# Performance work log

Measured on AMD Instinct MI355X. Metric: run time of the kernel, lower is better.

Reference implementation:

```python
import jax, jax.numpy as jnp
import numpy as np

# Mex config (matches init_kwargs)
B, C, H, W = 64, 64, 64, 64
BLK = (64, 3, 3)        # block over (C, H, W); spans all channels -> out_c = 1
STR = (64, 2, 2)
PAD = (0, 1, 1)
NI = 256                # num_instances
EPS = 1.0
SOFTMAX_MODE = False    # False -> mean (logsumexp - log k), True -> plain logsumexp


def setup_inputs() -> dict:
    key = jax.random.key(0)
    k1, k2 = jax.random.split(key)
    x = jax.random.normal(k1, (B, C, H, W), dtype=jnp.float32)
    kblk = BLK[0] * BLK[1] * BLK[2]
    # Dirichlet([1]*k) init == normalized exponentials; nregions = 1 (shared offsets)
    e = jax.random.exponential(k2, (1, NI, kblk), dtype=jnp.float32)
    offsets = (e / jnp.sum(e, axis=-1, keepdims=True)).reshape(1, NI, *BLK)
    return {"x": x, "offsets": offsets}


def _mex_forward(x, offsets):
    eps = jnp.float32(EPS)
    bc, bh, bw = BLK
    # im2col patch extraction: (B, C*bh*bw, OH, OW); feature dim ordered (c, fh, fw)
    patches = jax.lax.conv_general_dilated_patches(
        x, (bh, bw), (STR[1], STR[2]),
        [(PAD[1], PAD[1]), (PAD[2], PAD[2])],  # zero padding == blocks_out_of_bounds_value
        dimension_numbers=("NCHW", "OIHW", "NCHW"),
    )
    Bn, K, OH, OW = patches.shape  # K = bc*bh*bw = 576
    P = patches.transpose(0, 2, 3, 1).reshape(-1, K)  # (N, k), N = B*OH*OW
    O = offsets.reshape(NI, K)                         # single shared region

    # y_ni = (1/eps) * logsumexp_k( eps*(P_nk + O_ik) ) - log(k)/eps (mean mode)
    # exp-domain GEMM with max-shift for stability:
    Pe = eps * P
    Oe = eps * O
    mp = jnp.max(Pe, axis=1, keepdims=True)   # (N, 1)
    mo = jnp.max(Oe, axis=1, keepdims=True)   # (I, 1)
    S = jnp.exp(Pe - mp) @ jnp.exp(Oe - mo).T  # (N, I)
    y = (jnp.log(S) + mp + mo.T) / eps
    if not SOFTMAX_MODE:
        y = y - jnp.log(jnp.float32(K)) / eps
    # output: (B, num_instances * out_c, OH, OW) with out_c = 1
    return y.reshape(Bn, OH, OW, NI).transpose(0, 3, 1, 2)


def reference(x, offsets):
    return _mex_forward(x, offsets)
```

## Files before the change

### kernel.cpp

```cpp
#include <hip/hip_runtime.h>
#include <hip/hip_bf16.h>


typedef __bf16 bf16x8 __attribute__((ext_vector_type(8)));
typedef float  f32x4  __attribute__((ext_vector_type(4)));

__global__ void mex_prep_b(const float* __restrict__ off, __bf16* __restrict__ Bt) {
    const int i = blockIdx.x * 4 + (threadIdx.x >> 6);
    const int c = threadIdx.x & 63;
    const int c8 = c >> 3, j = c & 7;
    const int wv = i >> 6, nt = (i >> 4) & 3, t16 = i & 15;
    const int q  = c8 & 3;
    const float* oi = off + i * 576;
    #pragma unroll
    for (int p = 0; p < 9; ++p) {
        float v = oi[c * 9 + p];
        const int ks    = p * 2 + (c8 >> 2);
        const int chunk = (ks * 16 + wv * 4 + nt) * 64 + q * 16 + t16;
        Bt[chunk * 8 + j] = (__bf16)__expf(v);
    }
}

__global__ __launch_bounds__(256, 2) void mex_main(
        const float* __restrict__ x,
        const __bf16* __restrict__ Bt,
        float* __restrict__ out) {
    __shared__ bf16x8 lds8[2 * 2560];

    const int bid = blockIdx.x;
    const int wid  = ((bid & 7) << 6) | (bid >> 3);
    const int b    = wid >> 3;
    const int j2   = wid & 7;
    const int oh0a = j2 << 2;
    const int oh0b = oh0a + 2;
    const int tid  = threadIdx.x;
    const int wv   = tid >> 6;
    const int lane = tid & 63;

    bf16x8 one8;
    #pragma unroll
    for (int j = 0; j < 8; ++j) one8[j] = (__bf16)1.0f;

    if (oh0a == 0) {
        #pragma unroll
        for (int i = 0; i < 2; ++i) lds8[tid + i * 256] = one8;
    }

    const int wp  = tid & 31;
    const int w0  = wp << 1;
    const int c8  = tid >> 5;
    const int c8p = c8 ^ (wp & 7);
    const float* xb = x + ((size_t)b << 18) + w0;

    #pragma unroll
    for (int hl = 0; hl < 5; ++hl) {
        const int hg = 2 * oh0a - 1 + hl;
        if (hg >= 0) {
            const float* xp = xb + (hg << 6);
            float2 v[8];
            #pragma unroll
            for (int k = 0; k < 8; ++k)
                v[k] = *(const float2*)(xp + (((c8 << 3) + k) << 12));
            bf16x8 ca, cb;
            #pragma unroll
            for (int k = 0; k < 8; ++k) {
                ca[k] = (__bf16)__expf(v[k].x);
                cb[k] = (__bf16)__expf(v[k].y);
            }
            bf16x8* dst = lds8 + hl * 512 + w0 * 8 + c8p;
            dst[0] = ca;
            dst[8] = cb;
        }
    }

    float2 v1[40];
    #pragma unroll
    for (int hl = 0; hl < 5; ++hl) {
        const int hg = 2 * oh0b - 1 + hl;
        const float* xp = xb + (hg << 6);
        #pragma unroll
        for (int k = 0; k < 8; ++k)
            v1[hl * 8 + k] = *(const float2*)(xp + (((c8 << 3) + k) << 12));
    }

    const bf16x8* __restrict__ Btv = (const bf16x8*)Bt;
    const int wv4 = wv << 2;
    bf16x8 b0[4], b1[4];
    #pragma unroll
    for (int nt = 0; nt < 4; ++nt) {
        b0[nt] = Btv[(wv4 + nt) * 64 + lane];
        b1[nt] = Btv[(16 + wv4 + nt) * 64 + lane];
    }

    const int t16 = tid & 15;
    const int q   = (tid >> 4) & 3;
    int hb[4], wo2[4];
    #pragma unroll
    for (int mt = 0; mt < 4; ++mt) {
        const int m = mt * 16 + t16;
        wo2[mt] = (m & 31) << 1;
        hb[mt]  = (m >> 5) << 7;
    }
    const float lK = 6.356107660695891f;

    auto kloop = [&](const bf16x8* __restrict__ L, f32x4 (&acc)[4][4],
                     bf16x8 (&bc)[4], bf16x8 (&bn)[4]) {
        #pragma unroll
        for (int ks = 0; ks < 18; ++ks) {
            const int p  = ks >> 1;
            const int fh = (p * 11) >> 5;
            const int fw = p - fh * 3;
            const int ccq = ((ks & 1) << 2) + q;
            bf16x8 a[4];
            #pragma unroll
            for (int mt = 0; mt < 4; ++mt) {
                const int wc  = wo2[mt] + fw - 1;
                const int pad = wc < 0;
                const int wcl = pad ? 0 : wc;
                const int row = hb[mt] + fh * 64 + wcl;
                bf16x8 vv = L[row * 8 + (ccq ^ ((wcl >> 1) & 7))];
                a[mt] = pad ? one8 : vv;
            }
            bf16x8 b2[4];
            if (ks < 16) {
                #pragma unroll
                for (int nt = 0; nt < 4; ++nt)
                    b2[nt] = Btv[((ks + 2) * 16 + wv4 + nt) * 64 + lane];
            }
            #pragma unroll
            for (int mt = 0; mt < 4; ++mt)
                #pragma unroll
                for (int nt = 0; nt < 4; ++nt)
                    acc[mt][nt] = __builtin_amdgcn_mfma_f32_16x16x32_bf16(
                        a[mt], bc[nt], acc[mt][nt], 0, 0, 0);
            #pragma unroll
            for (int nt = 0; nt < 4; ++nt) { bc[nt] = bn[nt]; bn[nt] = b2[nt]; }
        }
    };

    auto epilogue = [&](f32x4 (&acc)[4][4], int oh0) {
        #pragma unroll
        for (int mt = 0; mt < 4; ++mt) {
            const int m   = mt * 16 + (q << 2);
            const int ohl = m >> 5;
            const int owi = m & 31;
            const int orow = (oh0 + ohl) * 32 + owi;
            #pragma unroll
            for (int nt = 0; nt < 4; ++nt) {
                const int inst = wv * 64 + nt * 16 + t16;
                f32x4 r;
                #pragma unroll
                for (int j = 0; j < 4; ++j)
                    r[j] = __logf(acc[mt][nt][j]) - lK;
                __builtin_nontemporal_store(
                    r, (f32x4*)(out + (((size_t)b * 256 + inst) * 1024 + orow)));
            }
        }
    };

    __syncthreads();

    f32x4 acc0[4][4];
    #pragma unroll
    for (int mt = 0; mt < 4; ++mt)
        #pragma unroll
        for (int nt = 0; nt < 4; ++nt) acc0[mt][nt] = (f32x4)(0.0f);
    kloop(lds8, acc0, b0, b1);

    #pragma unroll
    for (int hl = 0; hl < 5; ++hl) {
        bf16x8 ca, cb;
        #pragma unroll
        for (int k = 0; k < 8; ++k) {
            ca[k] = (__bf16)__expf(v1[hl * 8 + k].x);
            cb[k] = (__bf16)__expf(v1[hl * 8 + k].y);
        }
        bf16x8* dst = lds8 + 2560 + hl * 512 + w0 * 8 + c8p;
        dst[0] = ca;
        dst[8] = cb;
    }
    #pragma unroll
    for (int nt = 0; nt < 4; ++nt) {
        b0[nt] = Btv[(wv4 + nt) * 64 + lane];
        b1[nt] = Btv[(16 + wv4 + nt) * 64 + lane];
    }

    __syncthreads();

    epilogue(acc0, oh0a);

    f32x4 acc1[4][4];
    #pragma unroll
    for (int mt = 0; mt < 4; ++mt)
        #pragma unroll
        for (int nt = 0; nt < 4; ++nt) acc1[mt][nt] = (f32x4)(0.0f);
    kloop(lds8 + 2560, acc1, b0, b1);

    epilogue(acc1, oh0b);
}

extern "C" void kernel_launch(void* const* d_in, const int* in_sizes, int n_in,
                              void* d_out, int out_size, void* d_ws, size_t ws_size,
                              hipStream_t stream) {
    const float* x   = (const float*)d_in[0];
    const float* off = (const float*)d_in[1];
    float* out = (float*)d_out;
    __bf16* Bt = (__bf16*)d_ws;

    mex_prep_b<<<64, 256, 0, stream>>>(off, Bt);
    mex_main<<<512, 256, 0, stream>>>(x, Bt, out);
}
```

Before: 150.2 us.

## Double block size to 512 threads, splitting instances across 8 waves

```diff
diff --git a/kernel.cpp b/kernel.cpp
--- a/kernel.cpp
+++ b/kernel.cpp
@@ -3,25 +3,26 @@
 
 
 typedef __bf16 bf16x8 __attribute__((ext_vector_type(8)));
+typedef __bf16 bf16x4 __attribute__((ext_vector_type(4)));
 typedef float  f32x4  __attribute__((ext_vector_type(4)));
 
 __global__ void mex_prep_b(const float* __restrict__ off, __bf16* __restrict__ Bt) {
     const int i = blockIdx.x * 4 + (threadIdx.x >> 6);
     const int c = threadIdx.x & 63;
     const int c8 = c >> 3, j = c & 7;
-    const int wv = i >> 6, nt = (i >> 4) & 3, t16 = i & 15;
+    const int g  = i >> 4, t16 = i & 15;
     const int q  = c8 & 3;
     const float* oi = off + i * 576;
     #pragma unroll
     for (int p = 0; p < 9; ++p) {
         float v = oi[c * 9 + p];
         const int ks    = p * 2 + (c8 >> 2);
-        const int chunk = (ks * 16 + wv * 4 + nt) * 64 + q * 16 + t16;
+        const int chunk = (ks * 16 + g) * 64 + q * 16 + t16;
         Bt[chunk * 8 + j] = (__bf16)__expf(v);
     }
 }
 
-__global__ __launch_bounds__(256, 2) void mex_main(
+__global__ __launch_bounds__(512, 4) void mex_main(
         const float* __restrict__ x,
         const __bf16* __restrict__ Bt,
         float* __restrict__ out) {
@@ -41,15 +42,14 @@
     #pragma unroll
     for (int j = 0; j < 8; ++j) one8[j] = (__bf16)1.0f;
 
-    if (oh0a == 0) {
-        #pragma unroll
-        for (int i = 0; i < 2; ++i) lds8[tid + i * 256] = one8;
-    }
-
-    const int wp  = tid & 31;
-    const int w0  = wp << 1;
-    const int c8  = tid >> 5;
-    const int c8p = c8 ^ (wp & 7);
+    if (oh0a == 0) lds8[tid] = one8;
+
+    const int wp   = tid & 31;
+    const int w0   = wp << 1;
+    const int ch   = tid >> 5;
+    const int c8   = ch >> 1;
+    const int half = ch & 1;
+    const int c8p  = c8 ^ (wp & 7);
     const float* xb = x + ((size_t)b << 18) + w0;
 
     #pragma unroll
@@ -57,39 +57,38 @@
         const int hg = 2 * oh0a - 1 + hl;
         if (hg >= 0) {
             const float* xp = xb + (hg << 6);
-            float2 v[8];
-            #pragma unroll
-            for (int k = 0; k < 8; ++k)
-                v[k] = *(const float2*)(xp + (((c8 << 3) + k) << 12));
-            bf16x8 ca, cb;
-            #pragma unroll
-            for (int k = 0; k < 8; ++k) {
+            float2 v[4];
+            #pragma unroll
+            for (int k = 0; k < 4; ++k)
+                v[k] = *(const float2*)(xp + (((ch << 2) + k) << 12));
+            bf16x4 ca, cb;
+            #pragma unroll
+            for (int k = 0; k < 4; ++k) {
                 ca[k] = (__bf16)__expf(v[k].x);
                 cb[k] = (__bf16)__expf(v[k].y);
             }
-            bf16x8* dst = lds8 + hl * 512 + w0 * 8 + c8p;
-            dst[0] = ca;
-            dst[8] = cb;
-        }
-    }
-
-    float2 v1[40];
+            __bf16* bb = (__bf16*)(lds8 + hl * 512 + w0 * 8 + c8p) + (half << 2);
+            *(bf16x4*)bb        = ca;
+            *(bf16x4*)(bb + 64) = cb;
+        }
+    }
+
+    float2 v1[20];
     #pragma unroll
     for (int hl = 0; hl < 5; ++hl) {
-        const int hg = 2 * oh0b - 1 + hl;
-        const float* xp = xb + (hg << 6);
-        #pragma unroll
-        for (int k = 0; k < 8; ++k)
-            v1[hl * 8 + k] = *(const float2*)(xp + (((c8 << 3) + k) << 12));
+        const float* xp = xb + ((2 * oh0b - 1 + hl) << 6);
+        #pragma unroll
+        for (int k = 0; k < 4; ++k)
+            v1[hl * 4 + k] = *(const float2*)(xp + (((ch << 2) + k) << 12));
     }
 
     const bf16x8* __restrict__ Btv = (const bf16x8*)Bt;
-    const int wv4 = wv << 2;
-    bf16x8 b0[4], b1[4];
-    #pragma unroll
-    for (int nt = 0; nt < 4; ++nt) {
-        b0[nt] = Btv[(wv4 + nt) * 64 + lane];
-        b1[nt] = Btv[(16 + wv4 + nt) * 64 + lane];
+    const int g0 = wv << 1;
+    bf16x8 b0[2], b1[2];
+    #pragma unroll
+    for (int nt = 0; nt < 2; ++nt) {
+        b0[nt] = Btv[(g0 + nt) * 64 + lane];
+        b1[nt] = Btv[(16 + g0 + nt) * 64 + lane];
     }
 
     const int t16 = tid & 15;
@@ -103,8 +102,8 @@
     }
     const float lK = 6.356107660695891f;
 
-    auto kloop = [&](const bf16x8* __restrict__ L, f32x4 (&acc)[4][4],
-                     bf16x8 (&bc)[4], bf16x8 (&bn)[4]) {
+    auto kloop = [&](const bf16x8* __restrict__ L, f32x4 (&acc)[4][2],
+                     bf16x8 (&bc)[2], bf16x8 (&bn)[2]) {
         #pragma unroll
         for (int ks = 0; ks < 18; ++ks) {
             const int p  = ks >> 1;
@@ -121,24 +120,24 @@
                 bf16x8 vv = L[row * 8 + (ccq ^ ((wcl >> 1) & 7))];
                 a[mt] = pad ? one8 : vv;
             }
-            bf16x8 b2[4];
+            bf16x8 b2[2];
             if (ks < 16) {
                 #pragma unroll
-                for (int nt = 0; nt < 4; ++nt)
-                    b2[nt] = Btv[((ks + 2) * 16 + wv4 + nt) * 64 + lane];
+                for (int nt = 0; nt < 2; ++nt)
+                    b2[nt] = Btv[((ks + 2) * 16 + g0 + nt) * 64 + lane];
             }
             #pragma unroll
             for (int mt = 0; mt < 4; ++mt)
                 #pragma unroll
-                for (int nt = 0; nt < 4; ++nt)
+                for (int nt = 0; nt < 2; ++nt)
                     acc[mt][nt] = __builtin_amdgcn_mfma_f32_16x16x32_bf16(
                         a[mt], bc[nt], acc[mt][nt], 0, 0, 0);
             #pragma unroll
-            for (int nt = 0; nt < 4; ++nt) { bc[nt] = bn[nt]; bn[nt] = b2[nt]; }
+            for (int nt = 0; nt < 2; ++nt) { bc[nt] = bn[nt]; bn[nt] = b2[nt]; }
         }
     };
 
-    auto epilogue = [&](f32x4 (&acc)[4][4], int oh0) {
+    auto epilogue = [&](f32x4 (&acc)[4][2], int oh0) {
         #pragma unroll
         for (int mt = 0; mt < 4; ++mt) {
             const int m   = mt * 16 + (q << 2);
@@ -146,54 +145,53 @@
             const int owi = m & 31;
             const int orow = (oh0 + ohl) * 32 + owi;
             #pragma unroll
-            for (int nt = 0; nt < 4; ++nt) {
-                const int inst = wv * 64 + nt * 16 + t16;
+            for (int nt = 0; nt < 2; ++nt) {
+                const int inst = wv * 32 + nt * 16 + t16;
                 f32x4 r;
                 #pragma unroll
                 for (int j = 0; j < 4; ++j)
                     r[j] = __logf(acc[mt][nt][j]) - lK;
-                __builtin_nontemporal_store(
-                    r, (f32x4*)(out + (((size_t)b * 256 + inst) * 1024 + orow)));
+                *(f32x4*)(out + (((size_t)b * 256 + inst) * 1024 + orow)) = r;
             }
         }
     };
 
     __syncthreads();
 
-    f32x4 acc0[4][4];
+    f32x4 acc0[4][2];
     #pragma unroll
     for (int mt = 0; mt < 4; ++mt)
         #pragma unroll
-        for (int nt = 0; nt < 4; ++nt) acc0[mt][nt] = (f32x4)(0.0f);
+        for (int nt = 0; nt < 2; ++nt) acc0[mt][nt] = (f32x4)(0.0f);
     kloop(lds8, acc0, b0, b1);
 
     #pragma unroll
     for (int hl = 0; hl < 5; ++hl) {
-        bf16x8 ca, cb;
-        #pragma unroll
-        for (int k = 0; k < 8; ++k) {
-            ca[k] = (__bf16)__expf(v1[hl * 8 + k].x);
-            cb[k] = (__bf16)__expf(v1[hl * 8 + k].y);
-        }
-        bf16x8* dst = lds8 + 2560 + hl * 512 + w0 * 8 + c8p;
-        dst[0] = ca;
-        dst[8] = cb;
-    }
-    #pragma unroll
-    for (int nt = 0; nt < 4; ++nt) {
-        b0[nt] = Btv[(wv4 + nt) * 64 + lane];
-        b1[nt] = Btv[(16 + wv4 + nt) * 64 + lane];
+        bf16x4 ca, cb;
+        #pragma unroll
+        for (int k = 0; k < 4; ++k) {
+            ca[k] = (__bf16)__expf(v1[hl * 4 + k].x);
+            cb[k] = (__bf16)__expf(v1[hl * 4 + k].y);
+        }
+        __bf16* bb = (__bf16*)(lds8 + 2560 + hl * 512 + w0 * 8 + c8p) + (half << 2);
+        *(bf16x4*)bb        = ca;
+        *(bf16x4*)(bb + 64) = cb;
+    }
+    #pragma unroll
+    for (int nt = 0; nt < 2; ++nt) {
+        b0[nt] = Btv[(g0 + nt) * 64 + lane];
+        b1[nt] = Btv[(16 + g0 + nt) * 64 + lane];
     }
 
     __syncthreads();
 
     epilogue(acc0, oh0a);
 
-    f32x4 acc1[4][4];
+    f32x4 acc1[4][2];
     #pragma unroll
     for (int mt = 0; mt < 4; ++mt)
         #pragma unroll
-        for (int nt = 0; nt < 4; ++nt) acc1[mt][nt] = (f32x4)(0.0f);
+        for (int nt = 0; nt < 2; ++nt) acc1[mt][nt] = (f32x4)(0.0f);
     kloop(lds8 + 2560, acc1, b0, b1);
 
     epilogue(acc1, oh0b);
@@ -208,5 +206,5 @@
     __bf16* Bt = (__bf16*)d_ws;
 
     mex_prep_b<<<64, 256, 0, stream>>>(off, Bt);
-    mex_main<<<512, 256, 0, stream>>>(x, Bt, out);
+    mex_main<<<512, 512, 0, stream>>>(x, Bt, out);
 }
```

Result: no change. 150.8 us (+0.4%).

## Interleave second-tile input loads and first-tile epilogue stores into MFMA loops

Applied to the files above, without the earlier changes.

```diff
diff --git a/kernel.cpp b/kernel.cpp
--- a/kernel.cpp
+++ b/kernel.cpp
@@ -74,14 +74,7 @@
     }
 
     float2 v1[40];
-    #pragma unroll
-    for (int hl = 0; hl < 5; ++hl) {
-        const int hg = 2 * oh0b - 1 + hl;
-        const float* xp = xb + (hg << 6);
-        #pragma unroll
-        for (int k = 0; k < 8; ++k)
-            v1[hl * 8 + k] = *(const float2*)(xp + (((c8 << 3) + k) << 12));
-    }
+    const float* xc = xb + (((oh0b << 1) - 1) << 6) + ((size_t)c8 << 15);
 
     const bf16x8* __restrict__ Btv = (const bf16x8*)Bt;
     const int wv4 = wv << 2;
@@ -103,69 +96,58 @@
     }
     const float lK = 6.356107660695891f;
 
-    auto kloop = [&](const bf16x8* __restrict__ L, f32x4 (&acc)[4][4],
-                     bf16x8 (&bc)[4], bf16x8 (&bn)[4]) {
-        #pragma unroll
-        for (int ks = 0; ks < 18; ++ks) {
-            const int p  = ks >> 1;
-            const int fh = (p * 11) >> 5;
-            const int fw = p - fh * 3;
-            const int ccq = ((ks & 1) << 2) + q;
-            bf16x8 a[4];
-            #pragma unroll
-            for (int mt = 0; mt < 4; ++mt) {
-                const int wc  = wo2[mt] + fw - 1;
-                const int pad = wc < 0;
-                const int wcl = pad ? 0 : wc;
-                const int row = hb[mt] + fh * 64 + wcl;
-                bf16x8 vv = L[row * 8 + (ccq ^ ((wcl >> 1) & 7))];
-                a[mt] = pad ? one8 : vv;
+    f32x4 acc0[4][4], acc1[4][4];
+    #pragma unroll
+    for (int mt = 0; mt < 4; ++mt)
+        #pragma unroll
+        for (int nt = 0; nt < 4; ++nt) acc0[mt][nt] = (f32x4)(0.0f);
+
+    __syncthreads();
+
+    #pragma unroll
+    for (int ks = 0; ks < 18; ++ks) {
+        const int p  = ks >> 1;
+        const int fh = (p * 11) >> 5;
+        const int fw = p - fh * 3;
+        const int ccq = ((ks & 1) << 2) + q;
+        bf16x8 a[4];
+        #pragma unroll
+        for (int mt = 0; mt < 4; ++mt) {
+            const int wc  = wo2[mt] + fw - 1;
+            const int pad = wc < 0;
+            const int wcl = pad ? 0 : wc;
+            const int row = hb[mt] + fh * 64 + wcl;
+            bf16x8 vv = lds8[row * 8 + (ccq ^ ((wcl >> 1) & 7))];
+            a[mt] = pad ? one8 : vv;
+        }
+        bf16x8 b2[4];
+        if (ks < 16) {
+            #pragma unroll
+            for (int nt = 0; nt < 4; ++nt)
+                b2[nt] = Btv[((ks + 2) * 16 + wv4 + nt) * 64 + lane];
+        }
+        if (ks < 16) {
+            #pragma unroll
+            for (int u = 0; u < 2; ++u) {
+                const int k = 2 * ks + u;
+                v1[k] = *(const float2*)(xc + (k >> 3) * 64 + ((k & 7) << 12));
             }
-            bf16x8 b2[4];
-            if (ks < 16) {
-                #pragma unroll
-                for (int nt = 0; nt < 4; ++nt)
-                    b2[nt] = Btv[((ks + 2) * 16 + wv4 + nt) * 64 + lane];
+        } else {
+            #pragma unroll
+            for (int u = 0; u < 4; ++u) {
+                const int k = 32 + ((ks - 16) << 2) + u;
+                v1[k] = *(const float2*)(xc + (k >> 3) * 64 + ((k & 7) << 12));
             }
-            #pragma unroll
-            for (int mt = 0; mt < 4; ++mt)
-                #pragma unroll
-                for (int nt = 0; nt < 4; ++nt)
-                    acc[mt][nt] = __builtin_amdgcn_mfma_f32_16x16x32_bf16(
-                        a[mt], bc[nt], acc[mt][nt], 0, 0, 0);
-            #pragma unroll
-            for (int nt = 0; nt < 4; ++nt) { bc[nt] = bn[nt]; bn[nt] = b2[nt]; }
-        }
-    };
-
-    auto epilogue = [&](f32x4 (&acc)[4][4], int oh0) {
-        #pragma unroll
-        for (int mt = 0; mt < 4; ++mt) {
-            const int m   = mt * 16 + (q << 2);
-            const int ohl = m >> 5;
-            const int owi = m & 31;
-            const int orow = (oh0 + ohl) * 32 + owi;
-            #pragma unroll
-            for (int nt = 0; nt < 4; ++nt) {
-                const int inst = wv * 64 + nt * 16 + t16;
-                f32x4 r;
-                #pragma unroll
-                for (int j = 0; j < 4; ++j)
-                    r[j] = __logf(acc[mt][nt][j]) - lK;
-                __builtin_nontemporal_store(
-                    r, (f32x4*)(out + (((size_t)b * 256 + inst) * 1024 + orow)));
-            }
-        }
-    };
-
-    __syncthreads();
-
-    f32x4 acc0[4][4];
-    #pragma unroll
-    for (int mt = 0; mt < 4; ++mt)
-        #pragma unroll
-        for (int nt = 0; nt < 4; ++nt) acc0[mt][nt] = (f32x4)(0.0f);
-    kloop(lds8, acc0, b0, b1);
+        }
+        #pragma unroll
+        for (int mt = 0; mt < 4; ++mt)
+            #pragma unroll
+            for (int nt = 0; nt < 4; ++nt)
+                acc0[mt][nt] = __builtin_amdgcn_mfma_f32_16x16x32_bf16(
+                    a[mt], b0[nt], acc0[mt][nt], 0, 0, 0);
+        #pragma unroll
+        for (int nt = 0; nt < 4; ++nt) { b0[nt] = b1[nt]; b1[nt] = b2[nt]; }
+    }
 
     #pragma unroll
     for (int hl = 0; hl < 5; ++hl) {
@@ -184,19 +166,74 @@
         b0[nt] = Btv[(wv4 + nt) * 64 + lane];
         b1[nt] = Btv[(16 + wv4 + nt) * 64 + lane];
     }
+    #pragma unroll
+    for (int mt = 0; mt < 4; ++mt)
+        #pragma unroll
+        for (int nt = 0; nt < 4; ++nt) acc1[mt][nt] = (f32x4)(0.0f);
 
     __syncthreads();
 
-    epilogue(acc0, oh0a);
-
-    f32x4 acc1[4][4];
-    #pragma unroll
-    for (int mt = 0; mt < 4; ++mt)
-        #pragma unroll
-        for (int nt = 0; nt < 4; ++nt) acc1[mt][nt] = (f32x4)(0.0f);
-    kloop(lds8 + 2560, acc1, b0, b1);
-
-    epilogue(acc1, oh0b);
+    #pragma unroll
+    for (int ks = 0; ks < 18; ++ks) {
+        const int p  = ks >> 1;
+        const int fh = (p * 11) >> 5;
+        const int fw = p - fh * 3;
+        const int ccq = ((ks & 1) << 2) + q;
+        bf16x8 a[4];
+        #pragma unroll
+        for (int mt = 0; mt < 4; ++mt) {
+            const int wc  = wo2[mt] + fw - 1;
+            const int pad = wc < 0;
+            const int wcl = pad ? 0 : wc;
+            const int row = hb[mt] + fh * 64 + wcl;
+            bf16x8 vv = lds8[2560 + row * 8 + (ccq ^ ((wcl >> 1) & 7))];
+            a[mt] = pad ? one8 : vv;
+        }
+        bf16x8 b2[4];
+        if (ks < 16) {
+            #pragma unroll
+            for (int nt = 0; nt < 4; ++nt)
+                b2[nt] = Btv[((ks + 2) * 16 + wv4 + nt) * 64 + lane];
+        }
+        if (ks < 16) {
+            const int emt = ks >> 2, ent = ks & 3;
+            const int m    = emt * 16 + (q << 2);
+            const int ohl  = m >> 5;
+            const int owi  = m & 31;
+            const int orow = (oh0a + ohl) * 32 + owi;
+            const int inst = wv * 64 + ent * 16 + t16;
+            f32x4 r;
+            #pragma unroll
+            for (int j = 0; j < 4; ++j)
+                r[j] = __logf(acc0[emt][ent][j]) - lK;
+            *(f32x4*)(out + (((size_t)b * 256 + inst) * 1024 + orow)) = r;
+        }
+        #pragma unroll
+        for (int mt = 0; mt < 4; ++mt)
+            #pragma unroll
+            for (int nt = 0; nt < 4; ++nt)
+                acc1[mt][nt] = __builtin_amdgcn_mfma_f32_16x16x32_bf16(
+                    a[mt], b0[nt], acc1[mt][nt], 0, 0, 0);
+        #pragma unroll
+        for (int nt = 0; nt < 4; ++nt) { b0[nt] = b1[nt]; b1[nt] = b2[nt]; }
+    }
+
+    #pragma unroll
+    for (int mt = 0; mt < 4; ++mt) {
+        const int m   = mt * 16 + (q << 2);
+        const int ohl = m >> 5;
+        const int owi = m & 31;
+        const int orow = (oh0b + ohl) * 32 + owi;
+        #pragma unroll
+        for (int nt = 0; nt < 4; ++nt) {
+            const int inst = wv * 64 + nt * 16 + t16;
+            f32x4 r;
+            #pragma unroll
+            for (int j = 0; j < 4; ++j)
+                r[j] = __logf(acc1[mt][nt][j]) - lK;
+            *(f32x4*)(out + (((size_t)b * 256 + inst) * 1024 + orow)) = r;
+        }
+    }
 }
 
 extern "C" void kernel_launch(void* const* d_in, const int* in_sizes, int n_in,
```

Result: faster. 130.5 us (median of 2 runs) (-13.2%).
